# Kernel tuning notes

Measured on AMD Instinct MI355X. Metric: run time of the kernel, lower is better.

Reference implementation:

```python
import jax, jax.numpy as jnp
import numpy as np

N_NODES = 100000
IN_CH = 256
OUT_CH = 64
N_EDGES = 3200000


def setup_inputs() -> dict:
    key = jax.random.key(0)
    k1, k2, k3, k4 = jax.random.split(key, 4)
    x = jax.random.normal(k1, (N_NODES, IN_CH), dtype=jnp.float32)
    edge_index = jax.random.randint(k2, (2, N_EDGES), 0, N_NODES, dtype=jnp.int64)
    # GCNConv parameters (glorot-style init for W, zeros for bias as in PyG)
    W = jax.random.normal(k3, (IN_CH, OUT_CH), dtype=jnp.float32) / np.sqrt(IN_CH)
    b = jnp.zeros((OUT_CH,), dtype=jnp.float32)
    return {"x": x, "edge_index": edge_index, "W": W, "b": b}


def reference(x, edge_index, W, b):
    N = x.shape[0]
    # --- GCNConv: add self-loops, symmetric degree normalization ---
    loops = jnp.arange(N, dtype=edge_index.dtype)
    src = jnp.concatenate([edge_index[0], loops])  # [E+N]
    dst = jnp.concatenate([edge_index[1], loops])  # [E+N]
    # degree of each target node (edge weights = 1)
    deg = jax.ops.segment_sum(jnp.ones_like(dst, dtype=x.dtype), dst, num_segments=N)
    dinv = jnp.where(deg > 0, jax.lax.rsqrt(deg), 0.0)  # deg^{-1/2}
    norm = dinv[src] * dinv[dst]                        # [E+N]
    # linear transform first (PyG applies lin before propagate)
    h = x @ W                                           # [N, OUT_CH]
    msg = h[src] * norm[:, None]                        # gather + scale
    out = jax.ops.segment_sum(msg, dst, num_segments=N) + b  # scatter-add + bias
    # --- relu + log_softmax ---
    out = jax.nn.relu(out)
    return jax.nn.log_softmax(out, axis=-1)
```

## Files before the change

kernel.cpp:

```cpp
#include <hip/hip_runtime.h>
#include <cstddef>
#include <cstdint>

#define N_NODES 100000
#define IN_CH 256
#define OUT_CH 64
#define N_EDGES 3200000

#define BKT_SHIFT 7
#define BKT_R     128
#define K_BKT     782
#define BKT_CAP   6144
#define T_PART    8192
#define NBLK_PART ((N_EDGES + T_PART - 1) / T_PART)
#define NBLK_GEMM 512
#define N_TILES   (N_NODES / 16)

#define WS_FLAG_OFF   0
#define WS_GCNT_OFF   64
#define WS_DINV_OFF   4096
#define WS_NSE_OFF    404096
#define WS_EDG_OFF    1204224
#define WS_H_OFF      20422656
#define WS_NEED       33222656

#define WSF_DEG_OFF   4096
#define WSF_DINV_OFF  404096
#define WSF_H_OFF     804096

typedef __attribute__((ext_vector_type(8))) short bshort8;
typedef __attribute__((ext_vector_type(4))) float f32x4;
typedef __attribute__((ext_vector_type(4))) unsigned u32x4;

static __device__ __forceinline__ unsigned short f2bf(float f) {
    unsigned u = __builtin_bit_cast(unsigned, f);
    u += 0x7FFFu + ((u >> 16) & 1u);
    return (unsigned short)(u >> 16);
}
static __device__ __forceinline__ float bflo(unsigned u) {
    return __builtin_bit_cast(float, u << 16);
}
static __device__ __forceinline__ float bfhi(unsigned u) {
    return __builtin_bit_cast(float, u & 0xFFFF0000u);
}

__global__ void probe_kernel(const unsigned* __restrict__ ei, int* __restrict__ flag) {
    if (blockIdx.x == 0 && threadIdx.x == 0) {
        int all0 = 1;
        for (int i = 0; i < 16; ++i) all0 &= (ei[2 * i + 1] == 0u);
        *flag = all0;
    }
}

__device__ __forceinline__ int load_idx(const int* ei32, const long long* ei64,
                                        bool is64, long long pos) {
    return is64 ? (int)ei64[pos] : ei32[pos];
}

static __device__ __forceinline__ void gemm_body(char* smem, int gbid, int nblk,
                                                 const float* __restrict__ x,
                                                 const float* __restrict__ W,
                                                 unsigned short* __restrict__ hs) {
    unsigned short (*Wf)[4][64][8] = (unsigned short (*)[4][64][8])smem;
    const int tid = threadIdx.x;
    const int lane = tid & 63;
    const int wv = tid >> 6;

    for (int i = tid; i < 8 * 4 * 64 * 8; i += 256) {
        int kt = i >> 11;
        int rem = i & 2047;
        int ct = rem >> 9;
        int rem2 = rem & 511;
        int l = rem2 >> 3;
        int j = rem2 & 7;
        int kk = kt * 32 + (l >> 4) * 8 + j;
        int cc = ct * 16 + (l & 15);
        ((unsigned short*)Wf)[i] = f2bf(W[(size_t)kk * OUT_CH + cc]);
    }
    __syncthreads();

    const int r16 = lane & 15;
    const int q = lane >> 4;

    for (int t = gbid * 4 + wv; t < N_TILES; t += nblk * 4) {
        const int row0 = t * 16;
        const float* xrow = &x[(size_t)(row0 + r16) * IN_CH + q * 8];
        f32x4 acc[4] = {{0.f,0.f,0.f,0.f},{0.f,0.f,0.f,0.f},
                        {0.f,0.f,0.f,0.f},{0.f,0.f,0.f,0.f}};
        #pragma unroll
        for (int kt = 0; kt < 8; ++kt) {
            float4 x0 = *(const float4*)&xrow[kt * 32];
            float4 x1 = *(const float4*)&xrow[kt * 32 + 4];
            unsigned p0, p1, p2, p3;
            asm("v_cvt_pk_bf16_f32 %0, %1, %2" : "=v"(p0) : "v"(x0.x), "v"(x0.y));
            asm("v_cvt_pk_bf16_f32 %0, %1, %2" : "=v"(p1) : "v"(x0.z), "v"(x0.w));
            asm("v_cvt_pk_bf16_f32 %0, %1, %2" : "=v"(p2) : "v"(x1.x), "v"(x1.y));
            asm("v_cvt_pk_bf16_f32 %0, %1, %2" : "=v"(p3) : "v"(x1.z), "v"(x1.w));
            u32x4 au = {p0, p1, p2, p3};
            bshort8 af = __builtin_bit_cast(bshort8, au);
            #pragma unroll
            for (int ct = 0; ct < 4; ++ct) {
                bshort8 bf = *(const bshort8*)&Wf[kt][ct][lane][0];
                acc[ct] = __builtin_amdgcn_mfma_f32_16x16x32_bf16(af, bf, acc[ct], 0, 0, 0);
            }
        }
        #pragma unroll
        for (int ct = 0; ct < 4; ++ct) {
            #pragma unroll
            for (int r = 0; r < 4; ++r) {
                int row = row0 + q * 4 + r;
                hs[(size_t)row * OUT_CH + ct * 16 + r16] = f2bf(acc[ct][r]);
            }
        }
    }
}

__global__ __launch_bounds__(256) void part_gemm_kernel(const int* __restrict__ ei32,
                                                        const long long* __restrict__ ei64,
                                                        const int* __restrict__ flag,
                                                        unsigned* __restrict__ gcnt,
                                                        unsigned* __restrict__ edg,
                                                        const float* __restrict__ x,
                                                        const float* __restrict__ W,
                                                        unsigned short* __restrict__ hs) {
    __shared__ char smem[32768];
    const int bid = blockIdx.x;
    const int tid = threadIdx.x;

    if (bid < NBLK_PART) {
        unsigned* hist = (unsigned*)smem;
        unsigned* cur  = ((unsigned*)smem) + 1024;
        const bool is64 = (*flag != 0);
        const int start = bid * T_PART;
        const int end   = min(start + T_PART, N_EDGES);
        for (int k = tid; k < K_BKT; k += 256) hist[k] = 0u;
        __syncthreads();
        if (is64) {
            const longlong2* d2 = (const longlong2*)&ei64[N_EDGES];
            for (int i = (start >> 1) + tid; i < (end >> 1); i += 256) {
                longlong2 d = d2[i];
                atomicAdd(&hist[(int)d.x >> BKT_SHIFT], 1u);
                atomicAdd(&hist[(int)d.y >> BKT_SHIFT], 1u);
            }
        } else {
            const int2* d2 = (const int2*)&ei32[N_EDGES];
            for (int i = (start >> 1) + tid; i < (end >> 1); i += 256) {
                int2 d = d2[i];
                atomicAdd(&hist[d.x >> BKT_SHIFT], 1u);
                atomicAdd(&hist[d.y >> BKT_SHIFT], 1u);
            }
        }
        __syncthreads();
        for (int k = tid; k < K_BKT; k += 256) {
            unsigned c = hist[k];
            unsigned base = c ? atomicAdd(&gcnt[k], c) : 0u;
            cur[k] = base + (unsigned)k * BKT_CAP;
        }
        __syncthreads();
        if (is64) {
            const longlong2* s2 = (const longlong2*)&ei64[0];
            const longlong2* d2 = (const longlong2*)&ei64[N_EDGES];
            for (int i = (start >> 1) + tid; i < (end >> 1); i += 256) {
                longlong2 s = s2[i];
                longlong2 d = d2[i];
                unsigned p0 = atomicAdd(&cur[(int)d.x >> BKT_SHIFT], 1u);
                edg[p0] = (unsigned)s.x | ((unsigned)((int)d.x & (BKT_R - 1)) << 17);
                unsigned p1 = atomicAdd(&cur[(int)d.y >> BKT_SHIFT], 1u);
                edg[p1] = (unsigned)s.y | ((unsigned)((int)d.y & (BKT_R - 1)) << 17);
            }
        } else {
            const int2* s2 = (const int2*)&ei32[0];
            const int2* d2 = (const int2*)&ei32[N_EDGES];
            for (int i = (start >> 1) + tid; i < (end >> 1); i += 256) {
                int2 s = s2[i];
                int2 d = d2[i];
                unsigned p0 = atomicAdd(&cur[d.x >> BKT_SHIFT], 1u);
                edg[p0] = (unsigned)s.x | ((unsigned)(d.x & (BKT_R - 1)) << 17);
                unsigned p1 = atomicAdd(&cur[d.y >> BKT_SHIFT], 1u);
                edg[p1] = (unsigned)s.y | ((unsigned)(d.y & (BKT_R - 1)) << 17);
            }
        }
    } else {
        gemm_body(smem, bid - NBLK_PART, NBLK_GEMM, x, W, hs);
    }
}

__global__ __launch_bounds__(256) void gemm_only_kernel(const float* __restrict__ x,
                                                        const float* __restrict__ W,
                                                        unsigned short* __restrict__ hs) {
    __shared__ char smem[32768];
    gemm_body(smem, blockIdx.x, gridDim.x, x, W, hs);
}

__global__ __launch_bounds__(256) void sort2_kernel(unsigned* __restrict__ edg,
                                                    const unsigned* __restrict__ gcnt,
                                                    uint2* __restrict__ nse,
                                                    float* __restrict__ dinv) {
    __shared__ unsigned ld[BKT_CAP];
    __shared__ unsigned hist[BKT_R];
    __shared__ unsigned cur[BKT_R];
    const int k = blockIdx.x;
    const int t = threadIdx.x;
    const unsigned cnt = min(gcnt[k], (unsigned)BKT_CAP);
    const unsigned base = (unsigned)k * BKT_CAP;

    for (unsigned j = t; j < cnt; j += 256) ld[j] = edg[base + j];
    if (t < BKT_R) hist[t] = 0u;
    __syncthreads();
    for (unsigned j = t; j < cnt; j += 256)
        atomicAdd(&hist[ld[j] >> 17], 1u);
    __syncthreads();
    if (t < BKT_R) cur[t] = hist[t];
    __syncthreads();
    #pragma unroll
    for (int d = 1; d < BKT_R; d <<= 1) {
        unsigned x = (t < BKT_R && t >= d) ? cur[t - d] : 0u;
        __syncthreads();
        if (t < BKT_R) cur[t] += x;
        __syncthreads();
    }
    if (t < BKT_R) {
        unsigned mydeg = hist[t];
        unsigned start = base + cur[t] - mydeg;
        int n = k * BKT_R + t;
        if (n < N_NODES) {
            nse[n] = make_uint2(start, start + mydeg);
            dinv[n] = rsqrtf((float)(mydeg + 1u));
        }
        cur[t] = start;
    }
    __syncthreads();
    for (unsigned j = t; j < cnt; j += 256) {
        unsigned p = ld[j];
        unsigned pos = atomicAdd(&cur[p >> 17], 1u);
        edg[pos] = p & 0x1FFFF;
    }
}

__global__ __launch_bounds__(256) void reduce_kernel(const unsigned short* __restrict__ hs,
                                                     const float* __restrict__ dinv,
                                                     const uint2* __restrict__ nse,
                                                     const int* __restrict__ ssrc,
                                                     const float* __restrict__ b,
                                                     float* __restrict__ out) {
    const int n = blockIdx.x * 4 + (threadIdx.x >> 6);
    const int lane = threadIdx.x & 63;
    const int q = lane >> 4;
    const int l16 = lane & 15;
    if (n >= N_NODES) return;
    const uint2* h8 = (const uint2*)hs;
    const float dn = dinv[n];
    float a0 = 0.f, a1 = 0.f, a2 = 0.f, a3 = 0.f;
    {
        uint2 sv = h8[(size_t)n * 16 + l16];
        if (q == 0) {
            a0 = bflo(sv.x) * dn; a1 = bfhi(sv.x) * dn;
            a2 = bflo(sv.y) * dn; a3 = bfhi(sv.y) * dn;
        }
    }
    uint2 se = nse[n];
    unsigned j = se.x;
    const unsigned end = se.y;
    for (; j + 16 <= end; j += 16) {
        int s0 = ssrc[j + q];
        int s1 = ssrc[j + 4 + q];
        int s2 = ssrc[j + 8 + q];
        int s3 = ssrc[j + 12 + q];
        float f0 = dinv[s0], f1 = dinv[s1], f2 = dinv[s2], f3 = dinv[s3];
        uint2 v0 = h8[(size_t)s0 * 16 + l16];
        uint2 v1 = h8[(size_t)s1 * 16 + l16];
        uint2 v2 = h8[(size_t)s2 * 16 + l16];
        uint2 v3 = h8[(size_t)s3 * 16 + l16];
        a0 = fmaf(bflo(v0.x), f0, a0); a1 = fmaf(bfhi(v0.x), f0, a1);
        a2 = fmaf(bflo(v0.y), f0, a2); a3 = fmaf(bfhi(v0.y), f0, a3);
        a0 = fmaf(bflo(v1.x), f1, a0); a1 = fmaf(bfhi(v1.x), f1, a1);
        a2 = fmaf(bflo(v1.y), f1, a2); a3 = fmaf(bfhi(v1.y), f1, a3);
        a0 = fmaf(bflo(v2.x), f2, a0); a1 = fmaf(bfhi(v2.x), f2, a1);
        a2 = fmaf(bflo(v2.y), f2, a2); a3 = fmaf(bfhi(v2.y), f2, a3);
        a0 = fmaf(bflo(v3.x), f3, a0); a1 = fmaf(bfhi(v3.x), f3, a1);
        a2 = fmaf(bflo(v3.y), f3, a2); a3 = fmaf(bfhi(v3.y), f3, a3);
    }
    for (; j + 4 <= end; j += 4) {
        int s = ssrc[j + q];
        float f = dinv[s];
        uint2 v = h8[(size_t)s * 16 + l16];
        a0 = fmaf(bflo(v.x), f, a0); a1 = fmaf(bfhi(v.x), f, a1);
        a2 = fmaf(bflo(v.y), f, a2); a3 = fmaf(bfhi(v.y), f, a3);
    }
    unsigned rem = end - j;
    if ((unsigned)q < rem) {
        int s = ssrc[j + q];
        float f = dinv[s];
        uint2 v = h8[(size_t)s * 16 + l16];
        a0 = fmaf(bflo(v.x), f, a0); a1 = fmaf(bfhi(v.x), f, a1);
        a2 = fmaf(bflo(v.y), f, a2); a3 = fmaf(bfhi(v.y), f, a3);
    }
    a0 += __shfl_xor(a0, 16); a0 += __shfl_xor(a0, 32);
    a1 += __shfl_xor(a1, 16); a1 += __shfl_xor(a1, 32);
    a2 += __shfl_xor(a2, 16); a2 += __shfl_xor(a2, 32);
    a3 += __shfl_xor(a3, 16); a3 += __shfl_xor(a3, 32);
    float4 bb = ((const float4*)b)[l16];
    float v0 = fmaxf(fmaf(a0, dn, bb.x), 0.f);
    float v1 = fmaxf(fmaf(a1, dn, bb.y), 0.f);
    float v2 = fmaxf(fmaf(a2, dn, bb.z), 0.f);
    float v3 = fmaxf(fmaf(a3, dn, bb.w), 0.f);
    float m = fmaxf(fmaxf(v0, v1), fmaxf(v2, v3));
    #pragma unroll
    for (int o = 8; o; o >>= 1) m = fmaxf(m, __shfl_xor(m, o));
    float sum = expf(v0 - m) + expf(v1 - m) + expf(v2 - m) + expf(v3 - m);
    #pragma unroll
    for (int o = 8; o; o >>= 1) sum += __shfl_xor(sum, o);
    float ls = logf(sum);
    if (q == 0) {
        float4 r;
        r.x = (v0 - m) - ls; r.y = (v1 - m) - ls;
        r.z = (v2 - m) - ls; r.w = (v3 - m) - ls;
        *(float4*)&out[(size_t)n * OUT_CH + l16 * 4] = r;
    }
}

__global__ __launch_bounds__(256) void deg_kernel(const int* __restrict__ ei32,
                                                  const long long* __restrict__ ei64,
                                                  const int* __restrict__ flag,
                                                  unsigned* __restrict__ deg) {
    const bool is64 = (*flag != 0);
    int i = blockIdx.x * blockDim.x + threadIdx.x;
    const int stride = gridDim.x * blockDim.x;
    for (; i < N_EDGES; i += stride) {
        int d = load_idx(ei32, ei64, is64, (long long)N_EDGES + i);
        atomicAdd(&deg[d], 1u);
    }
}

__global__ __launch_bounds__(256) void dinv_kernel(const unsigned* __restrict__ deg,
                                                   float* __restrict__ dinv) {
    int i = blockIdx.x * blockDim.x + threadIdx.x;
    if (i < N_NODES) dinv[i] = rsqrtf((float)(deg[i] + 1u));
}

__global__ __launch_bounds__(256) void scatter_kernel(const int* __restrict__ ei32,
                                                      const long long* __restrict__ ei64,
                                                      const int* __restrict__ flag,
                                                      const unsigned short* __restrict__ hs,
                                                      const float* __restrict__ dinv,
                                                      float* __restrict__ out) {
    const bool is64 = (*flag != 0);
    const int lane = threadIdx.x & 63;
    int w = blockIdx.x * (blockDim.x >> 6) + (threadIdx.x >> 6);
    const int nw = gridDim.x * (blockDim.x >> 6);
    for (int e = w; e < N_EDGES; e += nw) {
        int s = load_idx(ei32, ei64, is64, e);
        int d = load_idx(ei32, ei64, is64, (long long)N_EDGES + e);
        unsigned short us = hs[(size_t)s * OUT_CH + lane];
        float hv = __builtin_bit_cast(float, (unsigned)us << 16);
        atomicAdd(&out[(size_t)d * OUT_CH + lane], hv * dinv[s] * dinv[d]);
    }
}

__global__ __launch_bounds__(256) void final_kernel(const unsigned short* __restrict__ hs,
                                                    const float* __restrict__ dinv,
                                                    const float* __restrict__ b,
                                                    float* __restrict__ out) {
    const int lane = threadIdx.x & 63;
    int w = blockIdx.x * (blockDim.x >> 6) + (threadIdx.x >> 6);
    const int nw = gridDim.x * (blockDim.x >> 6);
    const float bias = b[lane];
    for (int n = w; n < N_NODES; n += nw) {
        float di = dinv[n];
        unsigned short us = hs[(size_t)n * OUT_CH + lane];
        float hv = __builtin_bit_cast(float, (unsigned)us << 16);
        float v = out[(size_t)n * OUT_CH + lane] + hv * di * di + bias;
        v = fmaxf(v, 0.f);
        float m = v;
        #pragma unroll
        for (int o = 32; o; o >>= 1) m = fmaxf(m, __shfl_xor(m, o));
        float ex = expf(v - m);
        float sum = ex;
        #pragma unroll
        for (int o = 32; o; o >>= 1) sum += __shfl_xor(sum, o);
        out[(size_t)n * OUT_CH + lane] = (v - m) - logf(sum);
    }
}

extern "C" void kernel_launch(void* const* d_in, const int* in_sizes, int n_in,
                              void* d_out, int out_size, void* d_ws, size_t ws_size,
                              hipStream_t stream) {
    const float* x  = (const float*)d_in[0];
    const void*  ei = d_in[1];
    const float* W  = (const float*)d_in[2];
    const float* b  = (const float*)d_in[3];
    float* out = (float*)d_out;

    char* ws = (char*)d_ws;
    int* flag = (int*)(ws + WS_FLAG_OFF);

    const int* ei32       = (const int*)ei;
    const long long* ei64 = (const long long*)ei;

    probe_kernel<<<1, 64, 0, stream>>>((const unsigned*)ei, flag);

    if (ws_size >= (size_t)WS_NEED) {
        unsigned* gcnt = (unsigned*)(ws + WS_GCNT_OFF);
        float*    dinv = (float*)(ws + WS_DINV_OFF);
        uint2*    nse  = (uint2*)(ws + WS_NSE_OFF);
        unsigned* edg  = (unsigned*)(ws + WS_EDG_OFF);
        unsigned short* hs = (unsigned short*)(ws + WS_H_OFF);

        hipMemsetAsync(gcnt, 0, K_BKT * sizeof(unsigned), stream);
        part_gemm_kernel<<<NBLK_PART + NBLK_GEMM, 256, 0, stream>>>(
            ei32, ei64, flag, gcnt, edg, x, W, hs);
        sort2_kernel<<<K_BKT, 256, 0, stream>>>(edg, gcnt, nse, dinv);
        reduce_kernel<<<(N_NODES + 3) / 4, 256, 0, stream>>>(
            hs, dinv, nse, (const int*)edg, b, out);
    } else {
        unsigned* deg  = (unsigned*)(ws + WSF_DEG_OFF);
        float*    dinv = (float*)(ws + WSF_DINV_OFF);
        unsigned short* hs = (unsigned short*)(ws + WSF_H_OFF);
        hipMemsetAsync(deg, 0, (size_t)N_NODES * sizeof(unsigned), stream);
        hipMemsetAsync(d_out, 0, (size_t)out_size * sizeof(float), stream);
        deg_kernel<<<2048, 256, 0, stream>>>(ei32, ei64, flag, deg);
        dinv_kernel<<<(N_NODES + 255) / 256, 256, 0, stream>>>(deg, dinv);
        gemm_only_kernel<<<NBLK_GEMM, 256, 0, stream>>>(x, W, hs);
        scatter_kernel<<<2048, 256, 0, stream>>>(ei32, ei64, flag, hs, dinv, out);
        final_kernel<<<1024, 256, 0, stream>>>(hs, dinv, b, out);
    }
}
```

Baseline: 176.1 us.

## Move GEMM co-scheduling from partition kernel to bucket-sort kernel

The dense x@W GEMM blocks now share a launch with the per-bucket local sort instead of the edge partition pass. The partition kernel becomes standalone and runs with 512 threads per block. The aim is to overlap the compute-bound GEMM with the latency-bound sort, and to let the bandwidth-heavy partition pass use the whole GPU without competing GEMM blocks. The risk is that the sort blocks become stragglers, or that the partition kernel loses the earlier overlap.

```diff
diff --git a/kernel.cpp b/kernel.cpp
--- a/kernel.cpp
+++ b/kernel.cpp
@@ -115,73 +115,117 @@
     }
 }
 
-__global__ __launch_bounds__(256) void part_gemm_kernel(const int* __restrict__ ei32,
+__global__ __launch_bounds__(512) void partition_kernel(const int* __restrict__ ei32,
                                                         const long long* __restrict__ ei64,
                                                         const int* __restrict__ flag,
                                                         unsigned* __restrict__ gcnt,
-                                                        unsigned* __restrict__ edg,
-                                                        const float* __restrict__ x,
-                                                        const float* __restrict__ W,
-                                                        unsigned short* __restrict__ hs) {
+                                                        unsigned* __restrict__ edg) {
+    __shared__ unsigned hist[K_BKT];
+    __shared__ unsigned cur[K_BKT];
+    const bool is64 = (*flag != 0);
+    const int tid = threadIdx.x;
+    const int start = blockIdx.x * T_PART;
+    const int end   = min(start + T_PART, N_EDGES);
+    for (int k = tid; k < K_BKT; k += 512) hist[k] = 0u;
+    __syncthreads();
+    if (is64) {
+        const longlong2* d2 = (const longlong2*)&ei64[N_EDGES];
+        for (int i = (start >> 1) + tid; i < (end >> 1); i += 512) {
+            longlong2 d = d2[i];
+            atomicAdd(&hist[(int)d.x >> BKT_SHIFT], 1u);
+            atomicAdd(&hist[(int)d.y >> BKT_SHIFT], 1u);
+        }
+    } else {
+        const int2* d2 = (const int2*)&ei32[N_EDGES];
+        for (int i = (start >> 1) + tid; i < (end >> 1); i += 512) {
+            int2 d = d2[i];
+            atomicAdd(&hist[d.x >> BKT_SHIFT], 1u);
+            atomicAdd(&hist[d.y >> BKT_SHIFT], 1u);
+        }
+    }
+    __syncthreads();
+    for (int k = tid; k < K_BKT; k += 512) {
+        unsigned c = hist[k];
+        unsigned base = c ? atomicAdd(&gcnt[k], c) : 0u;
+        cur[k] = base + (unsigned)k * BKT_CAP;
+    }
+    __syncthreads();
+    if (is64) {
+        const longlong2* s2 = (const longlong2*)&ei64[0];
+        const longlong2* d2 = (const longlong2*)&ei64[N_EDGES];
+        for (int i = (start >> 1) + tid; i < (end >> 1); i += 512) {
+            longlong2 s = s2[i];
+            longlong2 d = d2[i];
+            unsigned p0 = atomicAdd(&cur[(int)d.x >> BKT_SHIFT], 1u);
+            edg[p0] = (unsigned)s.x | ((unsigned)((int)d.x & (BKT_R - 1)) << 17);
+            unsigned p1 = atomicAdd(&cur[(int)d.y >> BKT_SHIFT], 1u);
+            edg[p1] = (unsigned)s.y | ((unsigned)((int)d.y & (BKT_R - 1)) << 17);
+        }
+    } else {
+        const int2* s2 = (const int2*)&ei32[0];
+        const int2* d2 = (const int2*)&ei32[N_EDGES];
+        for (int i = (start >> 1) + tid; i < (end >> 1); i += 512) {
+            int2 s = s2[i];
+            int2 d = d2[i];
+            unsigned p0 = atomicAdd(&cur[d.x >> BKT_SHIFT], 1u);
+            edg[p0] = (unsigned)s.x | ((unsigned)(d.x & (BKT_R - 1)) << 17);
+            unsigned p1 = atomicAdd(&cur[d.y >> BKT_SHIFT], 1u);
+            edg[p1] = (unsigned)s.y | ((unsigned)(d.y & (BKT_R - 1)) << 17);
+        }
+    }
+}
+
+__global__ __launch_bounds__(256) void sortgemm_kernel(unsigned* __restrict__ edg,
+                                                       const unsigned* __restrict__ gcnt,
+                                                       uint2* __restrict__ nse,
+                                                       float* __restrict__ dinv,
+                                                       const float* __restrict__ x,
+                                                       const float* __restrict__ W,
+                                                       unsigned short* __restrict__ hs) {
     __shared__ char smem[32768];
     const int bid = blockIdx.x;
-    const int tid = threadIdx.x;
-
-    if (bid < NBLK_PART) {
-        unsigned* hist = (unsigned*)smem;
-        unsigned* cur  = ((unsigned*)smem) + 1024;
-        const bool is64 = (*flag != 0);
-        const int start = bid * T_PART;
-        const int end   = min(start + T_PART, N_EDGES);
-        for (int k = tid; k < K_BKT; k += 256) hist[k] = 0u;
+    if (bid < K_BKT) {
+        unsigned* ld   = (unsigned*)smem;
+        unsigned* hist = (unsigned*)(smem + 24576);
+        unsigned* cur  = (unsigned*)(smem + 25088);
+        const int k = bid;
+        const int t = threadIdx.x;
+        const unsigned cnt = min(gcnt[k], (unsigned)BKT_CAP);
+        const unsigned base = (unsigned)k * BKT_CAP;
+
+        for (unsigned j = t; j < cnt; j += 256) ld[j] = edg[base + j];
+        if (t < BKT_R) hist[t] = 0u;
         __syncthreads();
-        if (is64) {
-            const longlong2* d2 = (const longlong2*)&ei64[N_EDGES];
-            for (int i = (start >> 1) + tid; i < (end >> 1); i += 256) {
-                longlong2 d = d2[i];
-                atomicAdd(&hist[(int)d.x >> BKT_SHIFT], 1u);
-                atomicAdd(&hist[(int)d.y >> BKT_SHIFT], 1u);
+        for (unsigned j = t; j < cnt; j += 256)
+            atomicAdd(&hist[ld[j] >> 17], 1u);
+        __syncthreads();
+        if (t < BKT_R) cur[t] = hist[t];
+        __syncthreads();
+        #pragma unroll
+        for (int d = 1; d < BKT_R; d <<= 1) {
+            unsigned v = (t < BKT_R && t >= d) ? cur[t - d] : 0u;
+            __syncthreads();
+            if (t < BKT_R) cur[t] += v;
+            __syncthreads();
+        }
+        if (t < BKT_R) {
+            unsigned mydeg = hist[t];
+            unsigned start = base + cur[t] - mydeg;
+            int n = k * BKT_R + t;
+            if (n < N_NODES) {
+                nse[n] = make_uint2(start, start + mydeg);
+                dinv[n] = rsqrtf((float)(mydeg + 1u));
             }
-        } else {
-            const int2* d2 = (const int2*)&ei32[N_EDGES];
-            for (int i = (start >> 1) + tid; i < (end >> 1); i += 256) {
-                int2 d = d2[i];
-                atomicAdd(&hist[d.x >> BKT_SHIFT], 1u);
-                atomicAdd(&hist[d.y >> BKT_SHIFT], 1u);
-            }
+            cur[t] = start;
         }
         __syncthreads();
-        for (int k = tid; k < K_BKT; k += 256) {
-            unsigned c = hist[k];
-            unsigned base = c ? atomicAdd(&gcnt[k], c) : 0u;
-            cur[k] = base + (unsigned)k * BKT_CAP;
-        }
-        __syncthreads();
-        if (is64) {
-            const longlong2* s2 = (const longlong2*)&ei64[0];
-            const longlong2* d2 = (const longlong2*)&ei64[N_EDGES];
-            for (int i = (start >> 1) + tid; i < (end >> 1); i += 256) {
-                longlong2 s = s2[i];
-                longlong2 d = d2[i];
-                unsigned p0 = atomicAdd(&cur[(int)d.x >> BKT_SHIFT], 1u);
-                edg[p0] = (unsigned)s.x | ((unsigned)((int)d.x & (BKT_R - 1)) << 17);
-                unsigned p1 = atomicAdd(&cur[(int)d.y >> BKT_SHIFT], 1u);
-                edg[p1] = (unsigned)s.y | ((unsigned)((int)d.y & (BKT_R - 1)) << 17);
-            }
-        } else {
-            const int2* s2 = (const int2*)&ei32[0];
-            const int2* d2 = (const int2*)&ei32[N_EDGES];
-            for (int i = (start >> 1) + tid; i < (end >> 1); i += 256) {
-                int2 s = s2[i];
-                int2 d = d2[i];
-                unsigned p0 = atomicAdd(&cur[d.x >> BKT_SHIFT], 1u);
-                edg[p0] = (unsigned)s.x | ((unsigned)(d.x & (BKT_R - 1)) << 17);
-                unsigned p1 = atomicAdd(&cur[d.y >> BKT_SHIFT], 1u);
-                edg[p1] = (unsigned)s.y | ((unsigned)(d.y & (BKT_R - 1)) << 17);
-            }
+        for (unsigned j = t; j < cnt; j += 256) {
+            unsigned p = ld[j];
+            unsigned pos = atomicAdd(&cur[p >> 17], 1u);
+            edg[pos] = p & 0x1FFFF;
         }
     } else {
-        gemm_body(smem, bid - NBLK_PART, NBLK_GEMM, x, W, hs);
+        gemm_body(smem, bid - K_BKT, NBLK_GEMM, x, W, hs);
     }
 }
 
@@ -190,51 +234,6 @@
                                                         unsigned short* __restrict__ hs) {
     __shared__ char smem[32768];
     gemm_body(smem, blockIdx.x, gridDim.x, x, W, hs);
-}
-
-__global__ __launch_bounds__(256) void sort2_kernel(unsigned* __restrict__ edg,
-                                                    const unsigned* __restrict__ gcnt,
-                                                    uint2* __restrict__ nse,
-                                                    float* __restrict__ dinv) {
-    __shared__ unsigned ld[BKT_CAP];
-    __shared__ unsigned hist[BKT_R];
-    __shared__ unsigned cur[BKT_R];
-    const int k = blockIdx.x;
-    const int t = threadIdx.x;
-    const unsigned cnt = min(gcnt[k], (unsigned)BKT_CAP);
-    const unsigned base = (unsigned)k * BKT_CAP;
-
-    for (unsigned j = t; j < cnt; j += 256) ld[j] = edg[base + j];
-    if (t < BKT_R) hist[t] = 0u;
-    __syncthreads();
-    for (unsigned j = t; j < cnt; j += 256)
-        atomicAdd(&hist[ld[j] >> 17], 1u);
-    __syncthreads();
-    if (t < BKT_R) cur[t] = hist[t];
-    __syncthreads();
-    #pragma unroll
-    for (int d = 1; d < BKT_R; d <<= 1) {
-        unsigned x = (t < BKT_R && t >= d) ? cur[t - d] : 0u;
-        __syncthreads();
-        if (t < BKT_R) cur[t] += x;
-        __syncthreads();
-    }
-    if (t < BKT_R) {
-        unsigned mydeg = hist[t];
-        unsigned start = base + cur[t] - mydeg;
-        int n = k * BKT_R + t;
-        if (n < N_NODES) {
-            nse[n] = make_uint2(start, start + mydeg);
-            dinv[n] = rsqrtf((float)(mydeg + 1u));
-        }
-        cur[t] = start;
-    }
-    __syncthreads();
-    for (unsigned j = t; j < cnt; j += 256) {
-        unsigned p = ld[j];
-        unsigned pos = atomicAdd(&cur[p >> 17], 1u);
-        edg[pos] = p & 0x1FFFF;
-    }
 }
 
 __global__ __launch_bounds__(256) void reduce_kernel(const unsigned short* __restrict__ hs,
@@ -407,9 +406,9 @@
         unsigned short* hs = (unsigned short*)(ws + WS_H_OFF);
 
         hipMemsetAsync(gcnt, 0, K_BKT * sizeof(unsigned), stream);
-        part_gemm_kernel<<<NBLK_PART + NBLK_GEMM, 256, 0, stream>>>(
-            ei32, ei64, flag, gcnt, edg, x, W, hs);
-        sort2_kernel<<<K_BKT, 256, 0, stream>>>(edg, gcnt, nse, dinv);
+        partition_kernel<<<NBLK_PART, 512, 0, stream>>>(ei32, ei64, flag, gcnt, edg);
+        sortgemm_kernel<<<K_BKT + NBLK_GEMM, 256, 0, stream>>>(
+            edg, gcnt, nse, dinv, x, W, hs);
         reduce_kernel<<<(N_NODES + 3) / 4, 256, 0, stream>>>(
             hs, dinv, nse, (const int*)edg, b, out);
     } else {
```

After: 165.8 us. 1.06x faster.
